# Kernel tuning notes

Measured on AMD Instinct MI355X. Metric: run time of the kernel, lower is better.

The kernel has to match this reference:

```python
import jax, jax.numpy as jnp
import numpy as np

B, FG, ANT, D = 256, 4, 32, 1024   # batch, freq_groups, antennas, d_model
H, DK = 16, 64                      # n_heads, d_k; inner_dim = H*DK = 1024
INNER = H * DK


def setup_inputs() -> dict:
    key = jax.random.key(0)
    ks = jax.random.split(key, 17)
    s = 0.02
    inp = {"x": jax.random.normal(ks[0], (B, FG * ANT, D), dtype=jnp.float32)}
    names = ["ant_q", "ant_k", "ant_v", "ant_out", "freq_q", "freq_k", "freq_v", "freq_out"]
    for i, n in enumerate(names):
        # all layers are D->INNER or INNER->D; here D == INNER == 1024
        inp[n + "_w"] = jax.random.normal(ks[1 + 2 * i], (D, INNER), dtype=jnp.float32) * s
        inp[n + "_b"] = jnp.zeros((INNER,), dtype=jnp.float32)
    return inp


def _elu1(x):
    return jax.nn.elu(x) + 1.0


def _linear_attention(x, wq, bq, wk, bk, wv, bv):
    # x: (Baug, Lax, D)
    Baug, Lax, _ = x.shape
    Q = _elu1((x @ wq + bq).reshape(Baug, Lax, H, DK))
    K = _elu1((x @ wk + bk).reshape(Baug, Lax, H, DK))
    V = (x @ wv + bv).reshape(Baug, Lax, H, DK)
    KV = jnp.einsum('blhd,blhe->bhde', K, V)      # (Baug, H, DK, DK)
    out = jnp.einsum('blhd,bhde->blhe', Q, KV)    # (Baug, Lax, H, DK)
    return out.reshape(Baug, Lax, INNER)


def reference(x, ant_q_w, ant_q_b, ant_k_w, ant_k_b, ant_v_w, ant_v_b,
              ant_out_w, ant_out_b, freq_q_w, freq_q_b, freq_k_w, freq_k_b,
              freq_v_w, freq_v_b, freq_out_w, freq_out_b):
    # L == ANT*FG, no CLS token; dropout is identity (eval mode)
    grid_ant = x.reshape(B * FG, ANT, D)
    ant = _linear_attention(grid_ant, ant_q_w, ant_q_b, ant_k_w, ant_k_b, ant_v_w, ant_v_b)
    grid_ant = grid_ant + (ant @ ant_out_w + ant_out_b)
    # (B, FG, ANT, D) -> (B, ANT, FG, D)
    grid = grid_ant.reshape(B, FG, ANT, D).transpose(0, 2, 1, 3)
    grid_freq = grid.reshape(B * ANT, FG, D)
    frq = _linear_attention(grid_freq, freq_q_w, freq_q_b, freq_k_w, freq_k_b, freq_v_w, freq_v_b)
    grid_freq = grid_freq + (frq @ freq_out_w + freq_out_b)
    # back to (B, FG, ANT, D) -> (B, L, D)
    out = grid_freq.reshape(B, ANT, FG, D).transpose(0, 2, 1, 3).reshape(B, FG * ANT, D)
    return out
```

## Files before the change

### kernel.cpp

```cpp
#include <hip/hip_runtime.h>
#include <math.h>


#define MTOT 32768
#define DM 1024

using half8   = __attribute__((ext_vector_type(8))) _Float16;
using h2      = __attribute__((ext_vector_type(2))) _Float16;
using floatx4 = __attribute__((ext_vector_type(4))) float;

#define ACT_NONE 0
#define ACT_ELU1 1
#define REMAP_NONE 0
#define REMAP_A2F 1
#define REMAP_F2O 2

#define VMWAIT(n) asm volatile("s_waitcnt vmcnt(" #n ")" ::: "memory")
#define SBAR() do { __builtin_amdgcn_s_barrier(); \
                    __builtin_amdgcn_sched_barrier(0); } while (0)

__device__ __forceinline__ void gload16(const void* g, void* ldsp) {
  __builtin_amdgcn_global_load_lds(
      (const __attribute__((address_space(1))) unsigned int*)g,
      (__attribute__((address_space(3))) unsigned int*)ldsp, 16, 0, 0);
}

__device__ __forceinline__ float fdot2f(h2 a, h2 b, float c) {
#if __has_builtin(__builtin_amdgcn_fdot2)
  return __builtin_amdgcn_fdot2(a, b, c, false);
#else
  return fmaf((float)a[0], (float)b[0], fmaf((float)a[1], (float)b[1], c));
#endif
}

template<int ACT, int REMAP, bool RES, bool OF32, bool OF16>
__global__ __launch_bounds__(512, 2) void gemm_k(
    const _Float16* __restrict__ A, const _Float16* __restrict__ W,
    const float* __restrict__ bias, const _Float16* __restrict__ resid,
    float rs, float* __restrict__ Cf, _Float16* __restrict__ Ch,
    float sin_s, float sout_s)
{
  __shared__ __align__(16) char lds[147456];

  const int t = threadIdx.x, w = t >> 6, l = t & 63;
  const int bx = blockIdx.x;
  const int m0 = (((bx & 7) << 4) + (bx >> 3)) * 256;
  const int n0 = blockIdx.y * 128;
  const int lr = l & 15, ls = l >> 4;
  const int wrow = (w >> 1) * 64, wcol = (w & 1) * 64;

  const int trow = t >> 3;
  const int tsk  = ((t & 7) ^ (trow & 7)) * 8;
  char* const ldsw = lds + w * 1024;

  int aoff[2][4], boff[2][4];
#pragma unroll
  for (int kk = 0; kk < 2; ++kk)
#pragma unroll
    for (int m = 0; m < 4; ++m) {
      int ra = wrow + m * 16 + lr;
      aoff[kk][m] = ra * 128 + (((kk * 4 + ls) ^ (ra & 7)) << 4);
      int rb = wcol + m * 16 + lr;
      boff[kk][m] = rb * 128 + (((kk * 4 + ls) ^ (rb & 7)) << 4);
    }

  floatx4 acc[4][4];
#pragma unroll
  for (int m = 0; m < 4; ++m)
#pragma unroll
    for (int n = 0; n < 4; ++n) acc[m][n] = (floatx4)0.f;

  auto stage = [&](int kt, int p) {
    const int kb = kt * 64;
#pragma unroll
    for (int i = 0; i < 4; ++i)
      gload16(A + (size_t)(m0 + i * 64 + trow) * DM + kb + tsk,
              ldsw + p * 32768 + i * 8192);
#pragma unroll
    for (int i = 0; i < 2; ++i)
      gload16(W + (size_t)(n0 + i * 64 + trow) * DM + kb + tsk,
              ldsw + 98304 + p * 16384 + i * 8192);
  };

  auto compute = [&](int p) {
    const char* Ab = lds + p * 32768;
    const char* Bb = lds + 98304 + p * 16384;
#pragma unroll
    for (int kk = 0; kk < 2; ++kk) {
      half8 af[4], bf[4];
#pragma unroll
      for (int m = 0; m < 4; ++m) af[m] = *(const half8*)(Ab + aoff[kk][m]);
#pragma unroll
      for (int n = 0; n < 4; ++n) bf[n] = *(const half8*)(Bb + boff[kk][n]);
      __builtin_amdgcn_s_setprio(1);
#pragma unroll
      for (int m = 0; m < 4; ++m)
#pragma unroll
        for (int n = 0; n < 4; ++n)
          acc[m][n] =
              __builtin_amdgcn_mfma_f32_16x16x32_f16(af[m], bf[n], acc[m][n], 0, 0, 0);
      __builtin_amdgcn_s_setprio(0);
    }
  };

  stage(0, 0);
  stage(1, 1);
  for (int t2 = 0; t2 < 14; ++t2) {
    stage(t2 + 2, (t2 + 2) % 3);
    VMWAIT(12);
    SBAR();
    compute(t2 % 3);
    SBAR();
  }
  VMWAIT(6);  SBAR(); compute(2); SBAR();
  VMWAIT(0);  SBAR(); compute(0);

  float bb[4];
#pragma unroll
  for (int n = 0; n < 4; ++n) bb[n] = bias[n0 + wcol + n * 16 + lr];

#pragma unroll
  for (int m = 0; m < 4; ++m)
#pragma unroll
    for (int n = 0; n < 4; ++n)
#pragma unroll
      for (int j = 0; j < 4; ++j) {
        int rt = wrow + m * 16 + ls * 4 + j;
        int ct = wcol + n * 16 + lr;
        float v = acc[m][n][j] * sin_s + bb[n];
        if (RES) v += rs * (float)resid[(size_t)(m0 + rt) * DM + n0 + ct];
        if (ACT == ACT_ELU1) v = (v > 0.f) ? (v + 1.f) : expf(v);
        acc[m][n][j] = v;
      }
  if (RES && REMAP != REMAP_NONE) __syncthreads();

#pragma unroll
  for (int m = 0; m < 4; ++m)
#pragma unroll
    for (int n = 0; n < 4; ++n)
#pragma unroll
      for (int j = 0; j < 4; ++j) {
        int rt = wrow + m * 16 + ls * 4 + j;
        int ct = wcol + n * 16 + lr;
        int mg = m0 + rt, ng = n0 + ct;
        int srw;
        if (REMAP == REMAP_NONE) {
          srw = mg;
        } else if (REMAP == REMAP_A2F) {
          int b = mg >> 7, fg = (mg >> 5) & 3, ant = mg & 31;
          srw = b * 128 + ant * 4 + fg;
        } else {
          int b = mg >> 7, ant = (mg >> 2) & 31, fg = mg & 3;
          srw = b * 128 + fg * 32 + ant;
        }
        float v = acc[m][n][j];
        if (OF32) Cf[(size_t)srw * DM + ng] = v;
        if (OF16) Ch[(size_t)srw * DM + ng] = (_Float16)(v * sout_s);
      }
}

__global__ __launch_bounds__(256) void linattn32_k(
    _Float16* __restrict__ Q, const _Float16* __restrict__ K,
    const _Float16* __restrict__ V, float sout)
{
  __shared__ _Float16 Qs[32][64];
  __shared__ _Float16 Ks[32][64];
  __shared__ _Float16 Vs[32][64];
  __shared__ float Ss[32][33];

  const int g = blockIdx.x, h = blockIdx.y;
  const size_t base = (size_t)g * 32 * DM + h * 64;
  const int t = threadIdx.x;

  {
    const int row = t >> 3, ch = (t & 7) * 8;
    half8 q8 = *(const half8*)(Q + base + (size_t)row * DM + ch);
    half8 k8 = *(const half8*)(K + base + (size_t)row * DM + ch);
    half8 v8 = *(const half8*)(V + base + (size_t)row * DM + ch);
    *(half8*)&Qs[row][ch ^ ((row & 7) * 8)] = q8;
    *(half8*)&Ks[row][ch ^ (((row >> 2) & 7) * 8)] = k8;
    *(half8*)&Vs[row][ch] = v8;
  }
  __syncthreads();

  {
    const int tt = t >> 3, sg = t & 7;
    const int xq = (tt & 7) * 8, xk = sg * 8;
    float acc[4] = {};
#pragma unroll
    for (int jj = 0; jj < 32; ++jj) {
      h2 qq = *(const h2*)&Qs[tt][(2 * jj) ^ xq];
#pragma unroll
      for (int si = 0; si < 4; ++si) {
        h2 kk = *(const h2*)&Ks[sg * 4 + si][(2 * jj) ^ xk];
        acc[si] = fdot2f(qq, kk, acc[si]);
      }
    }
#pragma unroll
    for (int si = 0; si < 4; ++si) Ss[tt][sg * 4 + si] = acc[si];
  }
  __syncthreads();

  {
    const int tt = t >> 3, e0 = (t & 7) * 8;
    float o[8] = {};
#pragma unroll
    for (int s = 0; s < 32; ++s) {
      float sv = Ss[tt][s];
      half8 vv = *(const half8*)&Vs[s][e0];
#pragma unroll
      for (int e = 0; e < 8; ++e) o[e] = fmaf(sv, (float)vv[e], o[e]);
    }
    half8 r;
#pragma unroll
    for (int e = 0; e < 8; ++e) r[e] = (_Float16)(o[e] * sout);
    *(half8*)(Q + base + (size_t)tt * DM + e0) = r;
  }
}

__global__ __launch_bounds__(256) void linattn4_k(
    _Float16* __restrict__ Q, const _Float16* __restrict__ K,
    const _Float16* __restrict__ V, float sout)
{
  __shared__ _Float16 Qs[4][1024];
  __shared__ _Float16 Ks[4][1024];
  __shared__ _Float16 Vs[4][1024];
  __shared__ float Ss[16][4][5];

  const int g = blockIdx.x;
  const size_t base = (size_t)g * 4 * DM;
  const int t = threadIdx.x;

  {
    const int off = t * 16;
    const int row = off >> 10, col = off & 1023;
    const int h = col >> 6, d = col & 63, x = (h & 7) * 8;
    const int c0 = h * 64 + (d ^ x), c1 = h * 64 + ((d + 8) ^ x);
    half8 q0 = *(const half8*)(Q + base + off);
    half8 q1 = *(const half8*)(Q + base + off + 8);
    half8 k0 = *(const half8*)(K + base + off);
    half8 k1 = *(const half8*)(K + base + off + 8);
    half8 v0 = *(const half8*)(V + base + off);
    half8 v1 = *(const half8*)(V + base + off + 8);
    *(half8*)&Qs[row][c0] = q0; *(half8*)&Qs[row][c1] = q1;
    *(half8*)&Ks[row][c0] = k0; *(half8*)&Ks[row][c1] = k1;
    *(half8*)&Vs[row][c0] = v0; *(half8*)&Vs[row][c1] = v1;
  }
  __syncthreads();

  {
    const int h = t >> 4, tt = (t >> 2) & 3, s = t & 3;
    const int x = (h & 7) * 8;
    const _Float16* qp = &Qs[tt][h * 64];
    const _Float16* kp = &Ks[s][h * 64];
    float acc = 0.f;
#pragma unroll
    for (int jj = 0; jj < 32; ++jj) {
      int dd = (2 * jj) ^ x;
      acc = fdot2f(*(const h2*)(qp + dd), *(const h2*)(kp + dd), acc);
    }
    Ss[h][tt][s] = acc;
  }
  __syncthreads();

  {
    const int tt = t >> 6, cg = t & 63;
    const int h = cg >> 2, e0 = (cg & 3) * 16, x = (h & 7) * 8;
    const float* sp = Ss[h][tt];
    float o[16] = {};
#pragma unroll
    for (int s = 0; s < 4; ++s) {
      float sv = sp[s];
      half8 va = *(const half8*)&Vs[s][h * 64 + (e0 ^ x)];
      half8 vb = *(const half8*)&Vs[s][h * 64 + ((e0 + 8) ^ x)];
#pragma unroll
      for (int e = 0; e < 8; ++e) {
        o[e]     = fmaf(sv, (float)va[e], o[e]);
        o[e + 8] = fmaf(sv, (float)vb[e], o[e + 8]);
      }
    }
    half8 r0, r1;
#pragma unroll
    for (int e = 0; e < 8; ++e) {
      r0[e] = (_Float16)(o[e] * sout);
      r1[e] = (_Float16)(o[e + 8] * sout);
    }
    _Float16* dst = Q + base + (size_t)tt * DM + h * 64 + e0;
    *(half8*)dst = r0;
    *(half8*)(dst + 8) = r1;
  }
}

struct WPtrs { const float* p[8]; };

__global__ __launch_bounds__(256) void transpose_w8_k(
    WPtrs ws, _Float16* __restrict__ wt)
{
  __shared__ float tile[32][33];
  const float* W = ws.p[blockIdx.z];
  _Float16* Wt = wt + (size_t)DM * DM * blockIdx.z;
  const int tx = threadIdx.x & 31, ty = threadIdx.x >> 5;
  const int k0 = blockIdx.x * 32, n0 = blockIdx.y * 32;
#pragma unroll
  for (int r = 0; r < 4; ++r)
    tile[ty + r * 8][tx] = W[(size_t)(k0 + ty + r * 8) * DM + n0 + tx];
  __syncthreads();
#pragma unroll
  for (int r = 0; r < 4; ++r)
    Wt[(size_t)(n0 + ty + r * 8) * DM + k0 + tx] = (_Float16)tile[tx][ty + r * 8];
}

__global__ __launch_bounds__(256) void convf2h_k(
    const float* __restrict__ x, _Float16* __restrict__ xh, int n8)
{
  for (int i = blockIdx.x * blockDim.x + threadIdx.x; i < n8;
       i += gridDim.x * blockDim.x) {
    float4 a = ((const float4*)x)[i * 2];
    float4 b = ((const float4*)x)[i * 2 + 1];
    half8 h;
    h[0] = (_Float16)a.x; h[1] = (_Float16)a.y; h[2] = (_Float16)a.z; h[3] = (_Float16)a.w;
    h[4] = (_Float16)b.x; h[5] = (_Float16)b.y; h[6] = (_Float16)b.z; h[7] = (_Float16)b.w;
    ((half8*)xh)[i] = h;
  }
}

extern "C" void kernel_launch(void* const* d_in, const int* in_sizes, int n_in,
                              void* d_out, int out_size, void* d_ws, size_t ws_size,
                              hipStream_t stream)
{
  const float* x   = (const float*)d_in[0];
  WPtrs wp;
  for (int j = 0; j < 8; ++j) wp.p[j] = (const float*)d_in[1 + 2 * j];
  const float* aqb = (const float*)d_in[2];  const float* akb = (const float*)d_in[4];
  const float* avb = (const float*)d_in[6];  const float* aob = (const float*)d_in[8];
  const float* fqb = (const float*)d_in[10]; const float* fkb = (const float*)d_in[12];
  const float* fvb = (const float*)d_in[14]; const float* fob = (const float*)d_in[16];
  float* out = (float*)d_out;

  const size_t NE = (size_t)MTOT * DM;
  _Float16* xh = (_Float16*)d_ws;
  _Float16* Qh = xh + NE;
  _Float16* Kh = Qh + NE;
  _Float16* Vh = Kh + NE;
  _Float16* wt = Vh + NE;
  const size_t WSZ = (size_t)DM * DM;

  dim3 gg(MTOT / 256, DM / 128), gb(512), sb(256);

  convf2h_k<<<2048, sb, 0, stream>>>(x, xh, (int)(NE / 8));
  transpose_w8_k<<<dim3(32, 32, 8), sb, 0, stream>>>(wp, wt);

  const float S = 0.0625f;

  gemm_k<ACT_ELU1, REMAP_NONE, false, false, true><<<gg, gb, 0, stream>>>(
      xh, wt + WSZ * 0, aqb, nullptr, 0.f, nullptr, Qh, 1.f, 1.f);
  gemm_k<ACT_ELU1, REMAP_NONE, false, false, true><<<gg, gb, 0, stream>>>(
      xh, wt + WSZ * 1, akb, nullptr, 0.f, nullptr, Kh, 1.f, 1.f);
  gemm_k<ACT_NONE, REMAP_NONE, false, false, true><<<gg, gb, 0, stream>>>(
      xh, wt + WSZ * 2, avb, nullptr, 0.f, nullptr, Vh, 1.f, 1.f);
  linattn32_k<<<dim3(1024, 16), sb, 0, stream>>>(Qh, Kh, Vh, S);
  gemm_k<ACT_NONE, REMAP_A2F, true, false, true><<<gg, gb, 0, stream>>>(
      Qh, wt + WSZ * 3, aob, xh, 1.f, nullptr, xh, 16.f, S);

  gemm_k<ACT_ELU1, REMAP_NONE, false, false, true><<<gg, gb, 0, stream>>>(
      xh, wt + WSZ * 4, fqb, nullptr, 0.f, nullptr, Qh, 16.f, S);
  gemm_k<ACT_ELU1, REMAP_NONE, false, false, true><<<gg, gb, 0, stream>>>(
      xh, wt + WSZ * 5, fkb, nullptr, 0.f, nullptr, Kh, 16.f, S);
  gemm_k<ACT_NONE, REMAP_NONE, false, false, true><<<gg, gb, 0, stream>>>(
      xh, wt + WSZ * 6, fvb, nullptr, 0.f, nullptr, Vh, 16.f, S);
  linattn4_k<<<8192, sb, 0, stream>>>(Qh, Kh, Vh, S);
  gemm_k<ACT_NONE, REMAP_F2O, true, true, false><<<gg, gb, 0, stream>>>(
      Qh, wt + WSZ * 7, fob, xh, 16.f, out, nullptr, 65536.f, 1.f);
}
```

Before: 988.3 us.

## Enlarge GEMM tile to 256x256 with double-buffered LDS pipeline

Each GEMM block now computes a 256x256 output tile instead of 256x128, with every wave owning a 128x64 sub-tile (8x4 MFMA accumulators). The aim is more arithmetic per byte loaded from global memory and LDS. To fit in LDS, the three-stage prefetch ring becomes a two-stage double buffer (64 KB per stage). The costs are twice the accumulator registers, which risks spilling or losing occupancy under launch_bounds(512,2), a shallower prefetch depth, and half as many blocks in the grid.

```diff
diff --git a/kernel.cpp b/kernel.cpp
--- a/kernel.cpp
+++ b/kernel.cpp
@@ -40,61 +40,64 @@
     float rs, float* __restrict__ Cf, _Float16* __restrict__ Ch,
     float sin_s, float sout_s)
 {
-  __shared__ __align__(16) char lds[147456];
+  __shared__ __align__(16) char lds[131072];
 
   const int t = threadIdx.x, w = t >> 6, l = t & 63;
   const int bx = blockIdx.x;
   const int m0 = (((bx & 7) << 4) + (bx >> 3)) * 256;
-  const int n0 = blockIdx.y * 128;
+  const int n0 = blockIdx.y * 256;
   const int lr = l & 15, ls = l >> 4;
-  const int wrow = (w >> 1) * 64, wcol = (w & 1) * 64;
+  const int wrow = (w >> 2) * 128, wcol = (w & 3) * 64;
 
   const int trow = t >> 3;
   const int tsk  = ((t & 7) ^ (trow & 7)) * 8;
-  char* const ldsw = lds + w * 1024;
-
-  int aoff[2][4], boff[2][4];
-#pragma unroll
-  for (int kk = 0; kk < 2; ++kk)
-#pragma unroll
-    for (int m = 0; m < 4; ++m) {
+
+  int aoff[2][8], boff[2][4];
+#pragma unroll
+  for (int kk = 0; kk < 2; ++kk) {
+#pragma unroll
+    for (int m = 0; m < 8; ++m) {
       int ra = wrow + m * 16 + lr;
       aoff[kk][m] = ra * 128 + (((kk * 4 + ls) ^ (ra & 7)) << 4);
-      int rb = wcol + m * 16 + lr;
-      boff[kk][m] = rb * 128 + (((kk * 4 + ls) ^ (rb & 7)) << 4);
-    }
-
-  floatx4 acc[4][4];
-#pragma unroll
-  for (int m = 0; m < 4; ++m)
+    }
+#pragma unroll
+    for (int n = 0; n < 4; ++n) {
+      int rb = wcol + n * 16 + lr;
+      boff[kk][n] = 32768 + rb * 128 + (((kk * 4 + ls) ^ (rb & 7)) << 4);
+    }
+  }
+
+  floatx4 acc[8][4];
+#pragma unroll
+  for (int m = 0; m < 8; ++m)
 #pragma unroll
     for (int n = 0; n < 4; ++n) acc[m][n] = (floatx4)0.f;
 
-  auto stage = [&](int kt, int p) {
+  auto stage = [&](int kt, int s) {
     const int kb = kt * 64;
+    char* const base = lds + s * 65536 + w * 1024;
 #pragma unroll
     for (int i = 0; i < 4; ++i)
       gload16(A + (size_t)(m0 + i * 64 + trow) * DM + kb + tsk,
-              ldsw + p * 32768 + i * 8192);
-#pragma unroll
-    for (int i = 0; i < 2; ++i)
+              base + i * 8192);
+#pragma unroll
+    for (int i = 0; i < 4; ++i)
       gload16(W + (size_t)(n0 + i * 64 + trow) * DM + kb + tsk,
-              ldsw + 98304 + p * 16384 + i * 8192);
+              base + 32768 + i * 8192);
   };
 
-  auto compute = [&](int p) {
-    const char* Ab = lds + p * 32768;
-    const char* Bb = lds + 98304 + p * 16384;
+  auto compute = [&](int s) {
+    const char* Ab = lds + s * 65536;
 #pragma unroll
     for (int kk = 0; kk < 2; ++kk) {
-      half8 af[4], bf[4];
-#pragma unroll
-      for (int m = 0; m < 4; ++m) af[m] = *(const half8*)(Ab + aoff[kk][m]);
-#pragma unroll
-      for (int n = 0; n < 4; ++n) bf[n] = *(const half8*)(Bb + boff[kk][n]);
+      half8 af[8], bf[4];
+#pragma unroll
+      for (int m = 0; m < 8; ++m) af[m] = *(const half8*)(Ab + aoff[kk][m]);
+#pragma unroll
+      for (int n = 0; n < 4; ++n) bf[n] = *(const half8*)(Ab + boff[kk][n]);
       __builtin_amdgcn_s_setprio(1);
 #pragma unroll
-      for (int m = 0; m < 4; ++m)
+      for (int m = 0; m < 8; ++m)
 #pragma unroll
         for (int n = 0; n < 4; ++n)
           acc[m][n] =
@@ -104,23 +107,23 @@
   };
 
   stage(0, 0);
-  stage(1, 1);
-  for (int t2 = 0; t2 < 14; ++t2) {
-    stage(t2 + 2, (t2 + 2) % 3);
-    VMWAIT(12);
+  for (int t2 = 0; t2 < 15; ++t2) {
+    stage(t2 + 1, (t2 + 1) & 1);
+    VMWAIT(8);
     SBAR();
-    compute(t2 % 3);
+    compute(t2 & 1);
     SBAR();
   }
-  VMWAIT(6);  SBAR(); compute(2); SBAR();
-  VMWAIT(0);  SBAR(); compute(0);
+  VMWAIT(0);
+  SBAR();
+  compute(1);
 
   float bb[4];
 #pragma unroll
   for (int n = 0; n < 4; ++n) bb[n] = bias[n0 + wcol + n * 16 + lr];
 
 #pragma unroll
-  for (int m = 0; m < 4; ++m)
+  for (int m = 0; m < 8; ++m)
 #pragma unroll
     for (int n = 0; n < 4; ++n)
 #pragma unroll
@@ -135,7 +138,7 @@
   if (RES && REMAP != REMAP_NONE) __syncthreads();
 
 #pragma unroll
-  for (int m = 0; m < 4; ++m)
+  for (int m = 0; m < 8; ++m)
 #pragma unroll
     for (int n = 0; n < 4; ++n)
 #pragma unroll
@@ -345,7 +348,7 @@
   _Float16* wt = Vh + NE;
   const size_t WSZ = (size_t)DM * DM;
 
-  dim3 gg(MTOT / 256, DM / 128), gb(512), sb(256);
+  dim3 gg(MTOT / 256, DM / 256), gb(512), sb(256);
 
   convf2h_k<<<2048, sb, 0, stream>>>(x, xh, (int)(NE / 8));
   transpose_w8_k<<<dim3(32, 32, 8), sb, 0, stream>>>(wp, wt);
```

Result: faster. 834.6 us (-15.6%).

## Retile GEMM to 128x256 blocks with K=32 stages and smaller LDS

Applied to the files above, without the earlier changes.

The GEMM block tile changes from 256x128 to 128x256, and the K step per stage drops from 64 to 32. Total LDS per block shrinks from 144 KB to 72 KB, which lets launch bounds ask for four blocks per CU instead of two. A new swizzled LDS layout packs two rows per 128-byte line to suit the 32-wide K slices, and the pipeline now runs 32 shallower stages with adjusted vmcnt waits. The aim is higher occupancy and better latency hiding. The cost is more barriers per unit of work, possible register pressure under the tighter bound, and a different M-block swizzle.

```diff
diff --git a/kernel.cpp b/kernel.cpp
--- a/kernel.cpp
+++ b/kernel.cpp
@@ -34,35 +34,35 @@
 }
 
 template<int ACT, int REMAP, bool RES, bool OF32, bool OF16>
-__global__ __launch_bounds__(512, 2) void gemm_k(
+__global__ __launch_bounds__(512, 4) void gemm_k(
     const _Float16* __restrict__ A, const _Float16* __restrict__ W,
     const float* __restrict__ bias, const _Float16* __restrict__ resid,
     float rs, float* __restrict__ Cf, _Float16* __restrict__ Ch,
     float sin_s, float sout_s)
 {
-  __shared__ __align__(16) char lds[147456];
+  __shared__ __align__(16) char lds[73728];
 
   const int t = threadIdx.x, w = t >> 6, l = t & 63;
   const int bx = blockIdx.x;
-  const int m0 = (((bx & 7) << 4) + (bx >> 3)) * 256;
-  const int n0 = blockIdx.y * 128;
+  const int m0 = (((bx & 7) << 5) + (bx >> 3)) * 128;
+  const int n0 = blockIdx.y * 256;
   const int lr = l & 15, ls = l >> 4;
-  const int wrow = (w >> 1) * 64, wcol = (w & 1) * 64;
-
-  const int trow = t >> 3;
-  const int tsk  = ((t & 7) ^ (trow & 7)) * 8;
-  char* const ldsw = lds + w * 1024;
-
-  int aoff[2][4], boff[2][4];
-#pragma unroll
-  for (int kk = 0; kk < 2; ++kk)
-#pragma unroll
-    for (int m = 0; m < 4; ++m) {
-      int ra = wrow + m * 16 + lr;
-      aoff[kk][m] = ra * 128 + (((kk * 4 + ls) ^ (ra & 7)) << 4);
-      int rb = wcol + m * 16 + lr;
-      boff[kk][m] = rb * 128 + (((kk * 4 + ls) ^ (rb & 7)) << 4);
-    }
+  const int wrow = (w >> 2) * 64, wcol = (w & 3) * 64;
+
+  const int v    = (t & 7) ^ ((t >> 3) & 7);
+  const int arow = ((t >> 3) << 1) + (v >> 2);
+  const int akh  = (v & 3) * 8;
+  const int wloff = w * 1024;
+
+  int aoff[4], boff[4];
+#pragma unroll
+  for (int m = 0; m < 4; ++m) {
+    int ra = wrow + m * 16 + lr;
+    aoff[m] = (ra >> 1) * 128 + ((((ra & 1) << 2 | ls) ^ ((ra >> 1) & 7)) << 4);
+    int rb = wcol + m * 16 + lr;
+    boff[m] = 8192 + (rb >> 1) * 128 +
+              ((((rb & 1) << 2 | ls) ^ ((rb >> 1) & 7)) << 4);
+  }
 
   floatx4 acc[4][4];
 #pragma unroll
@@ -70,50 +70,42 @@
 #pragma unroll
     for (int n = 0; n < 4; ++n) acc[m][n] = (floatx4)0.f;
 
-  auto stage = [&](int kt, int p) {
-    const int kb = kt * 64;
-#pragma unroll
-    for (int i = 0; i < 4; ++i)
-      gload16(A + (size_t)(m0 + i * 64 + trow) * DM + kb + tsk,
-              ldsw + p * 32768 + i * 8192);
-#pragma unroll
-    for (int i = 0; i < 2; ++i)
-      gload16(W + (size_t)(n0 + i * 64 + trow) * DM + kb + tsk,
-              ldsw + 98304 + p * 16384 + i * 8192);
+  auto stage = [&](int kt, int s) {
+    const int kb = kt * 32;
+    char* const sb = lds + s * 24576;
+    gload16(A + (size_t)(m0 + arow) * DM + kb + akh, sb + wloff);
+    gload16(W + (size_t)(n0 + arow) * DM + kb + akh, sb + 8192 + wloff);
+    gload16(W + (size_t)(n0 + 128 + arow) * DM + kb + akh, sb + 16384 + wloff);
   };
 
-  auto compute = [&](int p) {
-    const char* Ab = lds + p * 32768;
-    const char* Bb = lds + 98304 + p * 16384;
-#pragma unroll
-    for (int kk = 0; kk < 2; ++kk) {
-      half8 af[4], bf[4];
-#pragma unroll
-      for (int m = 0; m < 4; ++m) af[m] = *(const half8*)(Ab + aoff[kk][m]);
-#pragma unroll
-      for (int n = 0; n < 4; ++n) bf[n] = *(const half8*)(Bb + boff[kk][n]);
-      __builtin_amdgcn_s_setprio(1);
-#pragma unroll
-      for (int m = 0; m < 4; ++m)
-#pragma unroll
-        for (int n = 0; n < 4; ++n)
-          acc[m][n] =
-              __builtin_amdgcn_mfma_f32_16x16x32_f16(af[m], bf[n], acc[m][n], 0, 0, 0);
-      __builtin_amdgcn_s_setprio(0);
-    }
+  auto compute = [&](int s) {
+    const char* sb = lds + s * 24576;
+    half8 af[4], bf[4];
+#pragma unroll
+    for (int m = 0; m < 4; ++m) af[m] = *(const half8*)(sb + aoff[m]);
+#pragma unroll
+    for (int n = 0; n < 4; ++n) bf[n] = *(const half8*)(sb + boff[n]);
+    __builtin_amdgcn_s_setprio(1);
+#pragma unroll
+    for (int m = 0; m < 4; ++m)
+#pragma unroll
+      for (int n = 0; n < 4; ++n)
+        acc[m][n] =
+            __builtin_amdgcn_mfma_f32_16x16x32_f16(af[m], bf[n], acc[m][n], 0, 0, 0);
+    __builtin_amdgcn_s_setprio(0);
   };
 
   stage(0, 0);
   stage(1, 1);
-  for (int t2 = 0; t2 < 14; ++t2) {
+  for (int t2 = 0; t2 < 30; ++t2) {
     stage(t2 + 2, (t2 + 2) % 3);
-    VMWAIT(12);
+    VMWAIT(6);
     SBAR();
     compute(t2 % 3);
     SBAR();
   }
-  VMWAIT(6);  SBAR(); compute(2); SBAR();
-  VMWAIT(0);  SBAR(); compute(0);
+  VMWAIT(3); SBAR(); compute(0); SBAR();
+  VMWAIT(0); SBAR(); compute(1);
 
   float bb[4];
 #pragma unroll
@@ -127,10 +119,10 @@
       for (int j = 0; j < 4; ++j) {
         int rt = wrow + m * 16 + ls * 4 + j;
         int ct = wcol + n * 16 + lr;
-        float v = acc[m][n][j] * sin_s + bb[n];
-        if (RES) v += rs * (float)resid[(size_t)(m0 + rt) * DM + n0 + ct];
-        if (ACT == ACT_ELU1) v = (v > 0.f) ? (v + 1.f) : expf(v);
-        acc[m][n][j] = v;
+        float v2 = acc[m][n][j] * sin_s + bb[n];
+        if (RES) v2 += rs * (float)resid[(size_t)(m0 + rt) * DM + n0 + ct];
+        if (ACT == ACT_ELU1) v2 = (v2 > 0.f) ? (v2 + 1.f) : expf(v2);
+        acc[m][n][j] = v2;
       }
   if (RES && REMAP != REMAP_NONE) __syncthreads();
 
@@ -153,9 +145,9 @@
           int b = mg >> 7, ant = (mg >> 2) & 31, fg = mg & 3;
           srw = b * 128 + fg * 32 + ant;
         }
-        float v = acc[m][n][j];
-        if (OF32) Cf[(size_t)srw * DM + ng] = v;
-        if (OF16) Ch[(size_t)srw * DM + ng] = (_Float16)(v * sout_s);
+        float v2 = acc[m][n][j];
+        if (OF32) Cf[(size_t)srw * DM + ng] = v2;
+        if (OF16) Ch[(size_t)srw * DM + ng] = (_Float16)(v2 * sout_s);
       }
 }
 
@@ -345,7 +337,7 @@
   _Float16* wt = Vh + NE;
   const size_t WSZ = (size_t)DM * DM;
 
-  dim3 gg(MTOT / 256, DM / 128), gb(512), sb(256);
+  dim3 gg(MTOT / 128, DM / 256), gb(512), sb(256);
 
   convf2h_k<<<2048, sb, 0, stream>>>(x, xh, (int)(NE / 8));
   transpose_w8_k<<<dim3(32, 32, 8), sb, 0, stream>>>(wp, wt);
```

Result: faster. 911.4 us (-7.8%).
